# Performance work log

Hardware: AMD Instinct MI355X
Metric: run time of the kernel (lower is better)

The kernel has to match this reference:

```python
import jax, jax.numpy as jnp
import numpy as np

B, DIM, HEADS, H, W = 4, 64, 8, 512, 512


def _conv(x, w, groups=1):
    # NCHW x, OIHW w, stride 1, SAME padding (padding=k//2 in torch)
    return jax.lax.conv_general_dilated(
        x, w, (1, 1), 'SAME', feature_group_count=groups,
        dimension_numbers=('NCHW', 'OIHW', 'NCHW'))


def _dwt_haar(x):
    # single-level orthonormal haar on even-sized NCHW input
    a = x[..., 0::2, 0::2]; b = x[..., 0::2, 1::2]
    c = x[..., 1::2, 0::2]; d = x[..., 1::2, 1::2]
    LL = (a + b + c + d) * 0.5
    LH = (-a - b + c + d) * 0.5
    HL = (-a + b - c + d) * 0.5
    HH = (a - b - c + d) * 0.5
    return LL, LH, HL, HH


def _idwt_haar(LL, LH, HL, HH):
    a = (LL - LH - HL + HH) * 0.5
    b = (LL - LH + HL - HH) * 0.5
    c = (LL + LH - HL - HH) * 0.5
    d = (LL + LH + HL + HH) * 0.5
    Bn, C, h, w = LL.shape
    even = jnp.stack([a, b], -1).reshape(Bn, C, h, 2 * w)  # rows 0::2
    odd = jnp.stack([c, d], -1).reshape(Bn, C, h, 2 * w)   # rows 1::2
    return jnp.stack([even, odd], -2).reshape(Bn, C, 2 * h, 2 * w)


def _l2norm(x, eps=1e-12):
    n = jnp.sqrt(jnp.sum(x * x, axis=-1, keepdims=True))
    return x / jnp.maximum(n, eps)


def setup_inputs() -> dict:
    key = jax.random.key(0)
    ks = jax.random.split(key, 8)
    def w(k, shape):
        fan_in = shape[1] * shape[2] * shape[3]
        return jax.random.normal(k, shape, jnp.float32) * (1.0 / np.sqrt(fan_in))
    return {
        'x': jax.random.normal(ks[0], (B, DIM, H, W), jnp.float32),
        'w_hc1': w(ks[1], (2 * DIM, DIM, 3, 3)),        # groups=2 over 2*dim channels
        'w_hc2': w(ks[2], (DIM, 2 * DIM, 1, 1)),
        'w_ho': w(ks[3], (3 * DIM, DIM, 3, 3)),          # groups=3 over 3*dim channels
        'w_qkv': w(ks[4], (3 * DIM, DIM, 1, 1)),
        'w_dw': w(ks[5], (3 * DIM, 1, 3, 3)),            # depthwise, groups=3*dim
        'w_proj': w(ks[6], (DIM, DIM, 1, 1)),
        'temperature': jnp.ones((HEADS, 1, 1), jnp.float32),
    }


def reference(x, w_hc1, w_hc2, w_ho, w_qkv, w_dw, w_proj, temperature):
    LL, LH, HL, HH = _dwt_haar(x)

    # high-frequency (LH,HL) filter branch
    hv = jnp.concatenate([LH, HL], axis=1)
    filter_hv = jax.nn.relu(_conv(jax.nn.relu(_conv(hv, w_hc1, groups=2)), w_hc2))

    # qkv from LL: 1x1 conv then depthwise 3x3
    qkv = _conv(_conv(LL, w_qkv), w_dw, groups=3 * DIM)
    q, k, v = jnp.split(qkv, 3, axis=1)
    b, c, h, w = q.shape
    v = v * filter_hv + v

    ch = c // HEADS
    q = q.reshape(b, HEADS, ch, h * w)
    k = k.reshape(b, HEADS, ch, h * w)
    v = v.reshape(b, HEADS, ch, h * w)
    q = _l2norm(q)
    k = _l2norm(k)

    attn = jnp.einsum('bhcn,bhdn->bhcd', q, k) * temperature  # [b,heads,ch,ch]
    attn = jax.nn.softmax(attn, axis=-1)
    out = jnp.einsum('bhcd,bhdn->bhcn', attn, v).reshape(b, c, h, w)
    out = _conv(out, w_proj)

    # high-frequency output branch
    yh = jax.nn.relu(_conv(jnp.concatenate([LH, HL, HH], axis=1), w_ho, groups=3))
    LH2, HL2, HH2 = jnp.split(yh, 3, axis=1)

    return _idwt_haar(out, LH2, HL2, HH2)
```

## Files before the change

kernel.cpp:

```cpp
#include <hip/hip_runtime.h>
#include <hip/hip_bf16.h>

#define BN 4
#define DIM 64
#define NHEADS 8
#define HH 256
#define WH 256
#define NP (HH*WH)
#define HF 512
#define WF 512

#define PD 258
#define PROW (PD*64)
#define PPLANE ((size_t)PD*PD*64)

typedef __attribute__((ext_vector_type(8))) short bfx8;
typedef __attribute__((ext_vector_type(8))) unsigned short u16x8;
typedef __attribute__((ext_vector_type(4))) unsigned short u16x4;
typedef __attribute__((ext_vector_type(4))) float f32x4;

static __device__ __forceinline__ short f2bf(float f) {
    unsigned u = __float_as_uint(f);
    unsigned r = (u + 0x7FFFu + ((u >> 16) & 1u)) >> 16;
    return (short)r;
}
static __device__ __forceinline__ float bfu(unsigned short u) {
    return __uint_as_float((unsigned)u << 16);
}

__global__ __launch_bounds__(256) void k_setup(unsigned short* __restrict__ tiled16,
                                               const float* __restrict__ w_ho,
                                               const float* __restrict__ w_hc1,
                                               const float* __restrict__ w_hc2,
                                               const float* __restrict__ w_qkv,
                                               short* __restrict__ wrHO,
                                               short* __restrict__ wrHC1,
                                               short* __restrict__ wrHC2,
                                               short* __restrict__ wrQKV) {
    int bx = blockIdx.x, tid = threadIdx.x;
    if (bx < 16) {
        char* base = (char*)(tiled16 + (size_t)bx * PPLANE);
        const int ROWB = PROW * 2;
        for (int k = tid; k < 8224; k += 256) {
            char* dst;
            if (k < 2064) dst = base + (size_t)k * 16;
            else if (k < 4128) dst = base + (size_t)257 * ROWB + (size_t)(k - 2064) * 16;
            else if (k < 6176) { int r = (k - 4128) >> 3, s = (k - 4128) & 7;
                dst = base + (size_t)(r + 1) * ROWB + (size_t)s * 16; }
            else { int r = (k - 6176) >> 3, s = (k - 6176) & 7;
                dst = base + (size_t)(r + 1) * ROWB + 257 * 128 + (size_t)s * 16; }
            *(uint4*)dst = (uint4){0, 0, 0, 0};
        }
        return;
    }
    if (bx < 16 + 432 + 288) {
        const float* w = (bx < 448) ? w_ho : w_hc1;
        short* wrep = (bx < 448) ? wrHO : wrHC1;
        int t = (bx - ((bx < 448) ? 16 : 448)) * 256 + tid;
        unsigned g   = (unsigned)t / 36864u;
        unsigned r1  = (unsigned)t % 36864u;
        unsigned tap = r1 / 4096u;
        unsigned r2  = r1 % 4096u;
        unsigned icb = r2 / 512u;
        unsigned r3  = r2 % 512u;
        unsigned oc  = r3 >> 3;
        unsigned j   = r3 & 7u;
        wrep[t] = f2bf(w[(((size_t)g * 64 + oc) * 64 + icb * 8u + j) * 9 + tap]);
        return;
    }
    if (bx < 16 + 432 + 288 + 32) {
        int t = (bx - 736) * 256 + tid;
        int j = t & 7, gr = t >> 3, o16 = gr & 15, X = gr >> 4;
        int icb = X % 16, oct = X / 16;
        wrHC2[t] = f2bf(w_hc2[(size_t)(oct * 16 + o16) * 128 + icb * 8 + j]);
        return;
    }
    {
        int t = (bx - 768) * 256 + tid;
        int j = t & 7, gr = t >> 3, o16 = gr & 15, X = gr >> 4;
        int icb = X % 8, oct = X / 8;
        wrQKV[t] = f2bf(w_qkv[(size_t)(oct * 16 + o16) * 64 + icb * 8 + j]);
    }
}

__global__ __launch_bounds__(256) void k_dwt(const float* __restrict__ x,
                                             unsigned short* __restrict__ tiled,
                                             unsigned short* __restrict__ llp) {
    __shared__ unsigned short lds[3 * 128 * 64] __attribute__((aligned(16)));
    const int tid = threadIdx.x;
    const int pid = blockIdx.x;
    const int b = blockIdx.y;
    const int y0 = (pid >> 4) * 8, x0 = (pid & 15) * 16;
    const int quad = tid & 127;
    const int qy = quad >> 4, qx = quad & 15;
    const int gy = y0 + qy, gx = x0 + qx;
    const int ich = tid >> 7;
    unsigned short* llb = llp + (size_t)b * PPLANE + ((size_t)(gy + 1) * PD + (gx + 1)) * 64;

#pragma unroll 4
    for (int it = 0; it < 16; ++it) {
        int ic = it * 4 + ich * 2;
        unsigned g = (((unsigned)(ic >> 3)) + (unsigned)gx + 2u * (unsigned)gy) & 7u;
        unsigned swz = (unsigned)quad * 64 + (g << 3) + (unsigned)(ic & 7);
        unsigned pk[3], pll;
#pragma unroll
        for (int s = 0; s < 2; ++s) {
            const float* px = x + (((size_t)(b * 64 + ic + s) * HF) + 2 * gy) * WF + 2 * gx;
            float2 e0 = *(const float2*)px;
            float2 e1 = *(const float2*)(px + WF);
            float a = e0.x, bb = e0.y, c = e1.x, d = e1.y;
            unsigned ll = (unsigned short)f2bf(( a + bb + c + d) * 0.5f);
            unsigned lh = (unsigned short)f2bf((-a - bb + c + d) * 0.5f);
            unsigned hl = (unsigned short)f2bf((-a + bb - c + d) * 0.5f);
            unsigned hh = (unsigned short)f2bf(( a - bb - c + d) * 0.5f);
            if (s == 0) { pll = ll; pk[0] = lh; pk[1] = hl; pk[2] = hh; }
            else { pll |= ll << 16; pk[0] |= lh << 16; pk[1] |= hl << 16; pk[2] |= hh << 16; }
        }
        *(unsigned*)&lds[swz]          = pk[0];
        *(unsigned*)&lds[8192 + swz]   = pk[1];
        *(unsigned*)&lds[16384 + swz]  = pk[2];
        *(unsigned*)&llb[(g << 3) + (unsigned)(ic & 7)] = pll;
    }
    __syncthreads();
#pragma unroll
    for (int it = 0; it < 12; ++it) {
        int cch = tid + it * 256;
        int p = cch >> 10, rem = cch & 1023;
        int row = rem >> 7, col = rem & 127;
        unsigned short* dst = tiled + ((size_t)(b * 3 + p) * PD + (y0 + row + 1)) * PROW
                                    + (size_t)(x0 + 1) * 64 + (size_t)col * 8;
        *(uint4*)dst = *(const uint4*)((const char*)lds + (size_t)cch * 16);
    }
}

template <int LAYOUT>
__global__ __launch_bounds__(256) void k_gconv3x3_mfma(const unsigned short* __restrict__ tiled,
                                                       const bfx8* __restrict__ wr,
                                                       unsigned short* __restrict__ out, int OC) {
    __shared__ short lds_in[324 * 64] __attribute__((aligned(16)));
    const int tid = threadIdx.x;
    const int l = tid & 63, wv = tid >> 6;
    const int tile = blockIdx.x;
    const int x0 = (tile & 15) * 16, y0 = (tile >> 4) * 16;
    const int g = blockIdx.y, b = blockIdx.z;
    const unsigned short* src = tiled + (size_t)(b * 3 + g) * PPLANE;

#pragma unroll
    for (int it = 0; it < 10; ++it) {
        int cch = it * 256 + tid;
        unsigned row = (unsigned)cch / 144u, col = (unsigned)cch % 144u;
        const unsigned short* ga = src + (size_t)(y0 + row) * PROW + (size_t)x0 * 64 + (size_t)col * 8;
        __builtin_amdgcn_global_load_lds(
            (const __attribute__((address_space(1))) void*)ga,
            (__attribute__((address_space(3))) void*)((char*)lds_in + (size_t)(it * 256 + wv * 64) * 16),
            16, 0, 0);
    }
    if (tid < 32) {
        int cch = 2560 + tid;
        unsigned row = (unsigned)cch / 144u, col = (unsigned)cch % 144u;
        const unsigned short* ga = src + (size_t)(y0 + row) * PROW + (size_t)x0 * 64 + (size_t)col * 8;
        *(uint4*)((char*)lds_in + (size_t)cch * 16) = *(const uint4*)ga;
    }
    __syncthreads();

    f32x4 acc[4][4];
#pragma unroll
    for (int i = 0; i < 4; ++i)
#pragma unroll
        for (int j = 0; j < 4; ++j) acc[i][j] = (f32x4){0.f, 0.f, 0.f, 0.f};

    const int lx = l & 15, lq = l >> 4;
#pragma unroll
    for (int c = 0; c < 2; ++c) {
        const int icb = c * 4 + lq;
#pragma unroll
        for (int tap = 0; tap < 9; ++tap) {
            const int dy = tap / 3, dx = tap % 3;
            const size_t wbase = ((size_t)(g * 9 + tap) * 8 + icb) * 64 + lx;
            bfx8 b0 = wr[wbase];
            bfx8 b1 = wr[wbase + 16];
            bfx8 b2 = wr[wbase + 32];
            bfx8 b3 = wr[wbase + 48];
#pragma unroll
            for (int pg = 0; pg < 4; ++pg) {
                int hy = wv * 4 + pg + dy, hx = lx + dx;
                int hp = hy * 18 + hx;
                const bfx8* ap = (const bfx8*)&lds_in[hp * 64 + (((icb + hx + 2 * hy + 5) & 7) << 3)];
                bfx8 a = *ap;
                acc[pg][0] = __builtin_amdgcn_mfma_f32_16x16x32_bf16(a, b0, acc[pg][0], 0, 0, 0);
                acc[pg][1] = __builtin_amdgcn_mfma_f32_16x16x32_bf16(a, b1, acc[pg][1], 0, 0, 0);
                acc[pg][2] = __builtin_amdgcn_mfma_f32_16x16x32_bf16(a, b2, acc[pg][2], 0, 0, 0);
                acc[pg][3] = __builtin_amdgcn_mfma_f32_16x16x32_bf16(a, b3, acc[pg][3], 0, 0, 0);
            }
        }
    }

#pragma unroll
    for (int pg = 0; pg < 4; ++pg) {
#pragma unroll
        for (int ocg = 0; ocg < 4; ++ocg) {
            f32x4 v = acc[pg][ocg];
            if (LAYOUT == 0) {
                unsigned short* op = out + ((size_t)(b * 256 + tile) * OC + g * 64 + ocg * 16 + lx) * 256
                                         + (wv * 4 + pg) * 16 + lq * 4;
                ushort4 s4;
                s4.x = (unsigned short)f2bf(fmaxf(v.x, 0.f));
                s4.y = (unsigned short)f2bf(fmaxf(v.y, 0.f));
                s4.z = (unsigned short)f2bf(fmaxf(v.z, 0.f));
                s4.w = (unsigned short)f2bf(fmaxf(v.w, 0.f));
                *(ushort4*)op = s4;
            } else {
                int icT = g * 64 + ocg * 16 + lx;
                int g16 = icT >> 3;
                unsigned short* tb = out + ((size_t)(b * 256 + tile) * 256) * 128;
                int innerb = (wv * 4 + pg) * 16 + lq * 4;
                float vr[4] = {v.x, v.y, v.z, v.w};
#pragma unroll
                for (int r = 0; r < 4; ++r) {
                    int inn = innerb + r;
                    tb[(size_t)inn * 128 + (((g16 + inn) & 15) << 3) + (icT & 7)] =
                        (unsigned short)f2bf(fmaxf(vr[r], 0.f));
                }
            }
        }
    }
}

template <int CIN, int OC, bool RELU>
__global__ __launch_bounds__(256) void k_conv1x1_mfma(const unsigned short* __restrict__ inT,
                                                      const bfx8* __restrict__ wr,
                                                      unsigned short* __restrict__ out) {
    constexpr int KB = CIN / 8;
    constexpr int KC = CIN / 32;
    constexpr int NOCT = OC / 16;
    __shared__ short ldsA[256 * CIN] __attribute__((aligned(16)));
    const int tid = threadIdx.x;
    const int l = tid & 63, wv = tid >> 6;
    const int tile = blockIdx.x, b = blockIdx.y;
    const unsigned short* src = inT + ((size_t)(b * 256 + tile) * 256) * CIN;
    constexpr int ITER = (256 * CIN / 8) / 256;
#pragma unroll
    for (int it = 0; it < ITER; ++it) {
        int cc = it * 256 + tid;
        __builtin_amdgcn_global_load_lds(
            (const __attribute__((address_space(1))) void*)(src + (size_t)cc * 8),
            (__attribute__((address_space(3))) void*)((char*)ldsA + (size_t)(it * 256 + wv * 64) * 16),
            16, 0, 0);
    }
    __syncthreads();

    const int lx = l & 15, lq = l >> 4;
    const int x0 = (tile & 15) * 16, y0 = (tile >> 4) * 16;
#pragma unroll
    for (int o4 = 0; o4 < NOCT / 4; ++o4) {
        f32x4 acc[4][4];
#pragma unroll
        for (int i = 0; i < 4; ++i)
#pragma unroll
            for (int j = 0; j < 4; ++j) acc[i][j] = (f32x4){0.f, 0.f, 0.f, 0.f};
#pragma unroll
        for (int c = 0; c < KC; ++c) {
            const int icb = c * 4 + lq;
            bfx8 bf[4];
#pragma unroll
            for (int ot = 0; ot < 4; ++ot)
                bf[ot] = wr[(size_t)(((o4 * 4 + ot) * KB + icb) * 16) + lx];
#pragma unroll
            for (int pg = 0; pg < 4; ++pg) {
                int inner = (wv * 4 + pg) * 16 + lx;
                const bfx8* ap = (const bfx8*)&ldsA[inner * CIN + (((icb + inner) & (KB - 1)) << 3)];
                bfx8 a = *ap;
                acc[pg][0] = __builtin_amdgcn_mfma_f32_16x16x32_bf16(a, bf[0], acc[pg][0], 0, 0, 0);
                acc[pg][1] = __builtin_amdgcn_mfma_f32_16x16x32_bf16(a, bf[1], acc[pg][1], 0, 0, 0);
                acc[pg][2] = __builtin_amdgcn_mfma_f32_16x16x32_bf16(a, bf[2], acc[pg][2], 0, 0, 0);
                acc[pg][3] = __builtin_amdgcn_mfma_f32_16x16x32_bf16(a, bf[3], acc[pg][3], 0, 0, 0);
            }
        }
#pragma unroll
        for (int pg = 0; pg < 4; ++pg)
#pragma unroll
            for (int ot = 0; ot < 4; ++ot) {
                int oc = (o4 * 4 + ot) * 16 + lx;
                unsigned short* op = out + ((size_t)b * OC + oc) * NP
                                         + (size_t)(y0 + wv * 4 + pg) * WH + x0 + lq * 4;
                f32x4 v = acc[pg][ot];
                ushort4 s4;
                s4.x = (unsigned short)f2bf(RELU ? fmaxf(v.x, 0.f) : v.x);
                s4.y = (unsigned short)f2bf(RELU ? fmaxf(v.y, 0.f) : v.y);
                s4.z = (unsigned short)f2bf(RELU ? fmaxf(v.z, 0.f) : v.z);
                s4.w = (unsigned short)f2bf(RELU ? fmaxf(v.w, 0.f) : v.w);
                *(ushort4*)op = s4;
            }
    }
}

__global__ __launch_bounds__(256) void k_qkv_fused(const unsigned short* __restrict__ llp,
                                                   const bfx8* __restrict__ wrq,
                                                   const float* __restrict__ wdw,
                                                   const unsigned short* __restrict__ filt,
                                                   unsigned short* __restrict__ vt,
                                                   float* __restrict__ praw,
                                                   float* __restrict__ praw2) {
    __shared__ short ldsA[336 * 64] __attribute__((aligned(16)));
    __shared__ short qsave[64 * 256] __attribute__((aligned(16)));
    __shared__ float ssq[2][4][64];
    const int tid = threadIdx.x;
    const int l = tid & 63, wv = tid >> 6;
    const int tile = blockIdx.x, b = blockIdx.y;
    const int x0 = (tile & 15) * 16, y0 = (tile >> 4) * 16;
    const unsigned short* src = llp + (size_t)b * PPLANE;

#pragma unroll
    for (int it = 0; it < 10; ++it) {
        int cch = it * 256 + tid;
        unsigned row = (unsigned)cch / 144u, col = (unsigned)cch % 144u;
        const unsigned short* ga = src + (size_t)(y0 + row) * PROW + (size_t)x0 * 64 + (size_t)col * 8;
        __builtin_amdgcn_global_load_lds(
            (const __attribute__((address_space(1))) void*)ga,
            (__attribute__((address_space(3))) void*)((char*)ldsA + (size_t)(it * 256 + wv * 64) * 16),
            16, 0, 0);
    }
    if (tid < 32) {
        int cch = 2560 + tid;
        unsigned row = (unsigned)cch / 144u, col = (unsigned)cch % 144u;
        const unsigned short* ga = src + (size_t)(y0 + row) * PROW + (size_t)x0 * 64 + (size_t)col * 8;
        *(uint4*)((char*)ldsA + (size_t)cch * 16) = *(const uint4*)ga;
    }
    __syncthreads();

    const int lx = l & 15, lq = l >> 4;
    bfx8 af[6][2];
#pragma unroll
    for (int m = 0; m < 6; ++m) {
        int mt = wv + 4 * m;
        if (mt < 21) {
            int hp = mt * 16 + lx;
            int hy = hp / 18, hx = hp - hy * 18;
#pragma unroll
            for (int kc = 0; kc < 2; ++kc) {
                int icb = kc * 4 + lq;
                af[m][kc] = *(const bfx8*)&ldsA[hp * 64 + (((icb + hx + 2 * hy + 5) & 7) << 3)];
            }
        }
    }
    __syncthreads();

    for (int g3 = 0; g3 < 3; ++g3) {
        bfx8 bw[2][4];
#pragma unroll
        for (int kc = 0; kc < 2; ++kc)
#pragma unroll
            for (int nt = 0; nt < 4; ++nt)
                bw[kc][nt] = wrq[(size_t)(((g3 * 4 + nt) * 8) + kc * 4 + lq) * 16 + lx];
#pragma unroll
        for (int m = 0; m < 6; ++m) {
            int mt = wv + 4 * m;
            if (mt < 21) {
                f32x4 acc[4];
#pragma unroll
                for (int nt = 0; nt < 4; ++nt) acc[nt] = (f32x4){0.f, 0.f, 0.f, 0.f};
#pragma unroll
                for (int kc = 0; kc < 2; ++kc) {
                    bfx8 a = af[m][kc];
#pragma unroll
                    for (int nt = 0; nt < 4; ++nt)
                        acc[nt] = __builtin_amdgcn_mfma_f32_16x16x32_bf16(a, bw[kc][nt], acc[nt], 0, 0, 0);
                }
#pragma unroll
                for (int nt = 0; nt < 4; ++nt) {
                    int ocl = nt * 16 + lx;
                    float vr[4] = {acc[nt].x, acc[nt].y, acc[nt].z, acc[nt].w};
#pragma unroll
                    for (int r = 0; r < 4; ++r) {
                        int hp2 = mt * 16 + lq * 4 + r;
                        int hy2 = hp2 / 18, hx2 = hp2 - hy2 * 18;
                        ldsA[hp2 * 64 + ((((ocl >> 3) + hx2 + 2 * hy2) & 7) << 3) + (ocl & 7)] =
                            f2bf(vr[r]);
                    }
                }
            }
        }
        __syncthreads();
        const int ch = l, chg = g3 * 64 + ch;
        float w9[9];
#pragma unroll
        for (int t = 0; t < 9; ++t) w9[t] = wdw[chg * 9 + t];
        float s2 = 0.f;
        u16x8 kpk[4][2];
#pragma unroll
        for (int yy = 0; yy < 4; ++yy) {
            int y = wv * 4 + yy;
            float ln[3][18];
#pragma unroll
            for (int hr = 0; hr < 3; ++hr) {
                int hy = y + hr;
#pragma unroll
                for (int hx = 0; hx < 18; ++hx)
                    ln[hr][hx] = bfu((unsigned short)ldsA[(hy * 18 + hx) * 64 +
                                     ((((ch >> 3) + hx + 2 * hy) & 7) << 3) + (ch & 7)]);
            }
            float ox[16];
#pragma unroll
            for (int xx = 0; xx < 16; ++xx) {
                float s = 0.f;
#pragma unroll
                for (int hr = 0; hr < 3; ++hr)
#pragma unroll
                    for (int dx = 0; dx < 3; ++dx)
                        s = fmaf(ln[hr][xx + dx], w9[hr * 3 + dx], s);
                ox[xx] = s;
            }
            if (g3 == 2) {
                const unsigned short* fp = filt + ((size_t)b * 64 + ch) * NP
                                                + (size_t)(y0 + y) * WH + x0;
                u16x8 f0 = *(const u16x8*)fp;
                u16x8 f1 = *(const u16x8*)(fp + 8);
#pragma unroll
                for (int k = 0; k < 8; ++k) ox[k]     = fmaf(ox[k],     bfu(f0[k]), ox[k]);
#pragma unroll
                for (int k = 0; k < 8; ++k) ox[8 + k] = fmaf(ox[8 + k], bfu(f1[k]), ox[8 + k]);
                unsigned short* vb = vt + ((size_t)(b * 256 + tile) * 256 + (size_t)y * 16) * 64 + ch;
#pragma unroll
                for (int xx = 0; xx < 16; ++xx) vb[xx * 64] = (unsigned short)f2bf(ox[xx]);
            } else {
#pragma unroll
                for (int xx = 0; xx < 16; ++xx) s2 = fmaf(ox[xx], ox[xx], s2);
                if (g3 == 0) {
#pragma unroll
                    for (int xx = 0; xx < 16; ++xx) {
                        int px = y * 16 + xx;
                        qsave[ch * 256 + ((((px >> 3) + ch) & 31) << 3) + (px & 7)] =
                            f2bf(ox[xx]);
                    }
                } else {
#pragma unroll
                    for (int xx = 0; xx < 8; ++xx)  kpk[yy][0][xx] = (unsigned short)f2bf(ox[xx]);
#pragma unroll
                    for (int xx = 0; xx < 8; ++xx)  kpk[yy][1][xx] = (unsigned short)f2bf(ox[8 + xx]);
                }
            }
        }
        if (g3 == 0) ssq[0][wv][ch] = s2;
        if (g3 == 1) {
            ssq[1][wv][ch] = s2;
            __syncthreads();
            short* kbuf = ldsA;
#pragma unroll
            for (int yy = 0; yy < 4; ++yy) {
                int y = wv * 4 + yy;
#pragma unroll
                for (int xx = 0; xx < 16; ++xx) {
                    int px = y * 16 + xx;
                    kbuf[ch * 256 + ((((px >> 3) + ch) & 31) << 3) + (px & 7)] =
                        (short)kpk[yy][xx >> 3][xx & 7];
                }
            }
            __syncthreads();
            f32x4 sacc[4];
#pragma unroll
            for (int t16 = 0; t16 < 4; ++t16) sacc[t16] = (f32x4){0.f, 0.f, 0.f, 0.f};
#pragma unroll
            for (int kc2 = 0; kc2 < 2; ++kc2) {
                int kc = wv * 2 + kc2;
#pragma unroll
                for (int t16 = 0; t16 < 4; ++t16) {
                    int chh = t16 * 16 + lx;
                    int go = chh * 256 + (((kc * 4 + lq + chh) & 31) << 3);
                    bfx8 aq = *(const bfx8*)&qsave[go];
                    bfx8 bk = *(const bfx8*)&kbuf[go];
                    sacc[t16] = __builtin_amdgcn_mfma_f32_16x16x32_bf16(aq, bk, sacc[t16], 0, 0, 0);
                }
            }
            __syncthreads();
            float* sred = (float*)qsave;
#pragma unroll
            for (int t16 = 0; t16 < 4; ++t16)
                *(f32x4*)&sred[((wv * 4 + t16) * 64 + l) * 4] = sacc[t16];
            __syncthreads();
            {
                int t16r = tid >> 6, lr = tid & 63;
                f32x4 s0 = *(const f32x4*)&sred[((0 * 4 + t16r) * 64 + lr) * 4];
                f32x4 s1 = *(const f32x4*)&sred[((1 * 4 + t16r) * 64 + lr) * 4];
                f32x4 s2r = *(const f32x4*)&sred[((2 * 4 + t16r) * 64 + lr) * 4];
                f32x4 s3 = *(const f32x4*)&sred[((3 * 4 + t16r) * 64 + lr) * 4];
                f32x4 sum = s0 + s1 + s2r + s3;
                *(f32x4*)&praw[(((size_t)(b * 256 + tile) * 4 + t16r) * 64 + lr) * 4] = sum;
                if (tid < 128) {
                    int which = tid >> 6, chh = tid & 63;
                    praw2[(size_t)(b * 256 + tile) * 128 + tid] =
                        ssq[which][0][chh] + ssq[which][1][chh] +
                        ssq[which][2][chh] + ssq[which][3][chh];
                }
            }
        }
        __syncthreads();
    }
}

__global__ __launch_bounds__(64) void k_attn_soft(const float* __restrict__ praw,
                                                  const float* __restrict__ praw2,
                                                  const float* __restrict__ temp,
                                                  float* __restrict__ attn) {
    int bhd = blockIdx.x;
    int b = bhd >> 3, hd = bhd & 7;
    int t = threadIdx.x, c = t >> 3, d = t & 7;
    int t16 = hd >> 1, half = hd & 1;
    int cl = half * 8 + c, dl = half * 8 + d;
    const float* pb = praw + ((size_t)(b * 256) * 4 + t16) * 256 + ((cl >> 2) * 16 + dl) * 4 + (cl & 3);
    const float* p2 = praw2 + (size_t)(b * 256) * 128;
    float s = 0.f, sq = 0.f, sk = 0.f;
    for (int tile = 0; tile < 256; ++tile) {
        s  += pb[(size_t)tile * 1024];
        sq += p2[(size_t)tile * 128 + hd * 8 + c];
        sk += p2[(size_t)tile * 128 + 64 + hd * 8 + d];
    }
    float nq = fmaxf(sqrtf(sq), 1e-12f);
    float nk = fmaxf(sqrtf(sk), 1e-12f);
    s = s / (nq * nk) * temp[hd];
    __shared__ float sm[64];
    __shared__ float se[64];
    sm[t] = s;
    __syncthreads();
    float mx = -1e30f;
#pragma unroll
    for (int dd = 0; dd < 8; ++dd) mx = fmaxf(mx, sm[c * 8 + dd]);
    float e = __expf(s - mx);
    se[t] = e;
    __syncthreads();
    float sum = 0.f;
#pragma unroll
    for (int dd = 0; dd < 8; ++dd) sum += se[c * 8 + dd];
    attn[(size_t)bhd * 64 + t] = e / sum;
}

__global__ __launch_bounds__(256) void k_prep_attn(const float* __restrict__ attn,
                                                   const float* __restrict__ wproj,
                                                   short* __restrict__ mrep) {
    int b = blockIdx.x, t = threadIdx.x;
    const float* ab = attn + (size_t)b * 512;
#pragma unroll
    for (int i = 0; i < 16; ++i) {
        int idx = t * 16 + i;
        int j = idx & 7, o16 = (idx >> 3) & 15, icb = (idx >> 7) & 7, oct = idx >> 10;
        int oc = oct * 16 + o16;
        float m = 0.f;
#pragma unroll
        for (int c8 = 0; c8 < 8; ++c8)
            m = fmaf(wproj[(size_t)oc * 64 + icb * 8 + c8], ab[icb * 64 + c8 * 8 + j], m);
        mrep[(size_t)b * 4096 + idx] = f2bf(m);
    }
}

__global__ __launch_bounds__(256) void k_attnout_idwt(const unsigned short* __restrict__ vt,
                                                      const bfx8* __restrict__ mrep,
                                                      const unsigned short* __restrict__ yht,
                                                      float* __restrict__ out) {
    const int tid = threadIdx.x;
    const int l = tid & 63, wv = tid >> 6;
    const int lx = l & 15, lq = l >> 4;
    const int tile = blockIdx.x, b = blockIdx.y;
    const int x0 = (tile & 15) * 16, y0 = (tile >> 4) * 16;
    const bfx8* vtb = (const bfx8*)(vt + (size_t)(b * 256 + tile) * 256 * 64);
    const bfx8* mb = mrep + (size_t)b * 512;

    bfx8 bw[2][4];
#pragma unroll
    for (int kc = 0; kc < 2; ++kc)
#pragma unroll
        for (int nt = 0; nt < 4; ++nt)
            bw[kc][nt] = mb[(nt * 8 + kc * 4 + lq) * 16 + lx];

    const unsigned short* yb = yht + (size_t)(b * 256 + tile) * 192 * 256;

#pragma unroll
    for (int pg = 0; pg < 4; ++pg) {
        const int mt = wv * 4 + pg;
        const int y = y0 + mt;
        bfx8 a0 = vtb[(mt * 16 + lx) * 8 + lq];
        bfx8 a1 = vtb[(mt * 16 + lx) * 8 + 4 + lq];

        f32x4 acc[4];
#pragma unroll
        for (int nt = 0; nt < 4; ++nt) acc[nt] = (f32x4){0.f, 0.f, 0.f, 0.f};
#pragma unroll
        for (int nt = 0; nt < 4; ++nt) {
            acc[nt] = __builtin_amdgcn_mfma_f32_16x16x32_bf16(a0, bw[0][nt], acc[nt], 0, 0, 0);
            acc[nt] = __builtin_amdgcn_mfma_f32_16x16x32_bf16(a1, bw[1][nt], acc[nt], 0, 0, 0);
        }
#pragma unroll
        for (int nt = 0; nt < 4; ++nt) {
            const int oc = nt * 16 + lx;
            const int inner = mt * 16 + lq * 4;
            const unsigned short* yp = yb + (size_t)oc * 256 + inner;
            u16x4 lh4 = *(const u16x4*)yp;
            u16x4 hl4 = *(const u16x4*)(yp + (size_t)64 * 256);
            u16x4 hh4 = *(const u16x4*)(yp + (size_t)128 * 256);
            float e0[8], e1[8];
#pragma unroll
            for (int r = 0; r < 4; ++r) {
                float s  = acc[nt][r];
                float LH = bfu(lh4[r]), HL = bfu(hl4[r]), HHv = bfu(hh4[r]);
                e0[2 * r]     = (s - LH - HL + HHv) * 0.5f;
                e0[2 * r + 1] = (s - LH + HL - HHv) * 0.5f;
                e1[2 * r]     = (s + LH - HL - HHv) * 0.5f;
                e1[2 * r + 1] = (s + LH + HL + HHv) * 0.5f;
            }
            float* o0 = out + ((size_t)(b * 64 + oc) * HF + 2 * y) * WF + 2 * (x0 + lq * 4);
            *(float4*)o0            = *(float4*)&e0[0];
            *(float4*)(o0 + 4)      = *(float4*)&e0[4];
            *(float4*)(o0 + WF)     = *(float4*)&e1[0];
            *(float4*)(o0 + WF + 4) = *(float4*)&e1[4];
        }
    }
}

extern "C" void kernel_launch(void* const* d_in, const int* in_sizes, int n_in,
                              void* d_out, int out_size, void* d_ws, size_t ws_size,
                              hipStream_t stream) {
    const float* x      = (const float*)d_in[0];
    const float* w_hc1  = (const float*)d_in[1];
    const float* w_hc2  = (const float*)d_in[2];
    const float* w_ho   = (const float*)d_in[3];
    const float* w_qkv  = (const float*)d_in[4];
    const float* w_dw   = (const float*)d_in[5];
    const float* w_proj = (const float*)d_in[6];
    const float* temp   = (const float*)d_in[7];
    float* out = (float*)d_out;

    char* base = (char*)d_ws;
    unsigned short* TILED = (unsigned short*)(base + 0);
    unsigned short* LLP   = (unsigned short*)(base + 102242304ULL);
    unsigned short* YH    = (unsigned short*)(base + 136323072ULL);
    unsigned short* T1T   = (unsigned short*)(base + 236986368ULL);
    unsigned short* FILT  = (unsigned short*)(base + 304095232ULL);
    unsigned short* VT    = (unsigned short*)(base + 337649664ULL);
    float*          PRAW  = (float*)(base + 371204096ULL);
    float*          PRAW2 = (float*)(base + 375398400ULL);
    float*          ATTN  = (float*)(base + 375922688ULL);
    short* WREP_HO  = (short*)(base + 375930880ULL);
    short* WREP_HC1 = (short*)(base + 376152064ULL);
    short* WREP_HC2 = (short*)(base + 376299520ULL);
    short* WREP_QKV = (short*)(base + 376315904ULL);
    short* MREP     = (short*)(base + 376340480ULL);

    k_setup<<<816, 256, 0, stream>>>(TILED, w_ho, w_hc1, w_hc2, w_qkv,
                                     WREP_HO, WREP_HC1, WREP_HC2, WREP_QKV);
    k_dwt<<<dim3(512, BN), 256, 0, stream>>>(x, TILED, LLP);
    k_gconv3x3_mfma<0><<<dim3(256, 3, BN), 256, 0, stream>>>(TILED, (const bfx8*)WREP_HO, YH, 192);
    k_gconv3x3_mfma<1><<<dim3(256, 2, BN), 256, 0, stream>>>(TILED, (const bfx8*)WREP_HC1, T1T, 128);
    k_conv1x1_mfma<128, 64, true><<<dim3(256, BN), 256, 0, stream>>>(T1T, (const bfx8*)WREP_HC2, FILT);
    k_qkv_fused<<<dim3(256, BN), 256, 0, stream>>>(LLP, (const bfx8*)WREP_QKV, w_dw, FILT,
                                                   VT, PRAW, PRAW2);
    k_attn_soft<<<32, 64, 0, stream>>>(PRAW, PRAW2, temp, ATTN);
    k_prep_attn<<<BN, 256, 0, stream>>>(ATTN, w_proj, MREP);
    k_attnout_idwt<<<dim3(256, BN), 256, 0, stream>>>(VT, (const bfx8*)MREP, YH, out);
}
```

Measured before the change: 563.7 us.

## Fuse high-frequency 3x3 grouped convs and 1x1 filter conv into one kernel

```diff
diff --git a/kernel.cpp b/kernel.cpp
--- a/kernel.cpp
+++ b/kernel.cpp
@@ -133,162 +133,189 @@
     }
 }
 
-template <int LAYOUT>
-__global__ __launch_bounds__(256) void k_gconv3x3_mfma(const unsigned short* __restrict__ tiled,
-                                                       const bfx8* __restrict__ wr,
-                                                       unsigned short* __restrict__ out, int OC) {
-    __shared__ short lds_in[324 * 64] __attribute__((aligned(16)));
+__global__ __launch_bounds__(256) void k_hi_fused(const unsigned short* __restrict__ tiled,
+                                                  const bfx8* __restrict__ wrHO,
+                                                  const bfx8* __restrict__ wrHC1,
+                                                  const bfx8* __restrict__ wrHC2,
+                                                  unsigned short* __restrict__ yh,
+                                                  unsigned short* __restrict__ filt) {
+    __shared__ short halo[324 * 64] __attribute__((aligned(16)));
+    __shared__ short t1A[256 * 64] __attribute__((aligned(16)));
     const int tid = threadIdx.x;
     const int l = tid & 63, wv = tid >> 6;
-    const int tile = blockIdx.x;
+    const int lx = l & 15, lq = l >> 4;
+    const int tile = blockIdx.x, b = blockIdx.y;
     const int x0 = (tile & 15) * 16, y0 = (tile >> 4) * 16;
-    const int g = blockIdx.y, b = blockIdx.z;
-    const unsigned short* src = tiled + (size_t)(b * 3 + g) * PPLANE;
-
-#pragma unroll
-    for (int it = 0; it < 10; ++it) {
-        int cch = it * 256 + tid;
-        unsigned row = (unsigned)cch / 144u, col = (unsigned)cch % 144u;
-        const unsigned short* ga = src + (size_t)(y0 + row) * PROW + (size_t)x0 * 64 + (size_t)col * 8;
-        __builtin_amdgcn_global_load_lds(
-            (const __attribute__((address_space(1))) void*)ga,
-            (__attribute__((address_space(3))) void*)((char*)lds_in + (size_t)(it * 256 + wv * 64) * 16),
-            16, 0, 0);
-    }
-    if (tid < 32) {
-        int cch = 2560 + tid;
-        unsigned row = (unsigned)cch / 144u, col = (unsigned)cch % 144u;
-        const unsigned short* ga = src + (size_t)(y0 + row) * PROW + (size_t)x0 * 64 + (size_t)col * 8;
-        *(uint4*)((char*)lds_in + (size_t)cch * 16) = *(const uint4*)ga;
-    }
-    __syncthreads();
-
-    f32x4 acc[4][4];
-#pragma unroll
-    for (int i = 0; i < 4; ++i)
-#pragma unroll
-        for (int j = 0; j < 4; ++j) acc[i][j] = (f32x4){0.f, 0.f, 0.f, 0.f};
-
-    const int lx = l & 15, lq = l >> 4;
-#pragma unroll
-    for (int c = 0; c < 2; ++c) {
-        const int icb = c * 4 + lq;
-#pragma unroll
-        for (int tap = 0; tap < 9; ++tap) {
-            const int dy = tap / 3, dx = tap % 3;
-            const size_t wbase = ((size_t)(g * 9 + tap) * 8 + icb) * 64 + lx;
-            bfx8 b0 = wr[wbase];
-            bfx8 b1 = wr[wbase + 16];
-            bfx8 b2 = wr[wbase + 32];
-            bfx8 b3 = wr[wbase + 48];
+    const int order[3] = {0, 2, 1};
+
+#pragma unroll
+    for (int ph = 0; ph < 3; ++ph) {
+        const int g = order[ph];
+        const unsigned short* src = tiled + (size_t)(b * 3 + g) * PPLANE;
+#pragma unroll
+        for (int it = 0; it < 10; ++it) {
+            int cch = it * 256 + tid;
+            unsigned row = (unsigned)cch / 144u, col = (unsigned)cch % 144u;
+            const unsigned short* ga = src + (size_t)(y0 + row) * PROW + (size_t)x0 * 64 + (size_t)col * 8;
+            __builtin_amdgcn_global_load_lds(
+                (const __attribute__((address_space(1))) void*)ga,
+                (__attribute__((address_space(3))) void*)((char*)halo + (size_t)(it * 256 + wv * 64) * 16),
+                16, 0, 0);
+        }
+        if (tid < 32) {
+            int cch = 2560 + tid;
+            unsigned row = (unsigned)cch / 144u, col = (unsigned)cch % 144u;
+            const unsigned short* ga = src + (size_t)(y0 + row) * PROW + (size_t)x0 * 64 + (size_t)col * 8;
+            *(uint4*)((char*)halo + (size_t)cch * 16) = *(const uint4*)ga;
+        }
+        __syncthreads();
+
+        {
+            f32x4 acc[4][4];
+#pragma unroll
+            for (int i = 0; i < 4; ++i)
+#pragma unroll
+                for (int j = 0; j < 4; ++j) acc[i][j] = (f32x4){0.f, 0.f, 0.f, 0.f};
+#pragma unroll
+            for (int c = 0; c < 2; ++c) {
+                const int icb = c * 4 + lq;
+#pragma unroll
+                for (int tap = 0; tap < 9; ++tap) {
+                    const int dy = tap / 3, dx = tap % 3;
+                    const size_t wbase = ((size_t)(g * 9 + tap) * 8 + icb) * 64 + lx;
+                    bfx8 b0 = wrHO[wbase];
+                    bfx8 b1 = wrHO[wbase + 16];
+                    bfx8 b2 = wrHO[wbase + 32];
+                    bfx8 b3 = wrHO[wbase + 48];
+#pragma unroll
+                    for (int pg = 0; pg < 4; ++pg) {
+                        int hy = wv * 4 + pg + dy, hx = lx + dx;
+                        int hp = hy * 18 + hx;
+                        bfx8 a = *(const bfx8*)&halo[hp * 64 + (((icb + hx + 2 * hy + 5) & 7) << 3)];
+                        acc[pg][0] = __builtin_amdgcn_mfma_f32_16x16x32_bf16(a, b0, acc[pg][0], 0, 0, 0);
+                        acc[pg][1] = __builtin_amdgcn_mfma_f32_16x16x32_bf16(a, b1, acc[pg][1], 0, 0, 0);
+                        acc[pg][2] = __builtin_amdgcn_mfma_f32_16x16x32_bf16(a, b2, acc[pg][2], 0, 0, 0);
+                        acc[pg][3] = __builtin_amdgcn_mfma_f32_16x16x32_bf16(a, b3, acc[pg][3], 0, 0, 0);
+                    }
+                }
+            }
+#pragma unroll
+            for (int pg = 0; pg < 4; ++pg)
+#pragma unroll
+                for (int ocg = 0; ocg < 4; ++ocg) {
+                    f32x4 v = acc[pg][ocg];
+                    unsigned short* op = yh + ((size_t)(b * 256 + tile) * 192 + g * 64 + ocg * 16 + lx) * 256
+                                            + (wv * 4 + pg) * 16 + lq * 4;
+                    ushort4 s4;
+                    s4.x = (unsigned short)f2bf(fmaxf(v.x, 0.f));
+                    s4.y = (unsigned short)f2bf(fmaxf(v.y, 0.f));
+                    s4.z = (unsigned short)f2bf(fmaxf(v.z, 0.f));
+                    s4.w = (unsigned short)f2bf(fmaxf(v.w, 0.f));
+                    *(ushort4*)op = s4;
+                }
+        }
+
+        if (ph != 1) {
+            f32x4 tacc[4][4];
+#pragma unroll
+            for (int i = 0; i < 4; ++i)
+#pragma unroll
+                for (int j = 0; j < 4; ++j) tacc[i][j] = (f32x4){0.f, 0.f, 0.f, 0.f};
+#pragma unroll
+            for (int c = 0; c < 2; ++c) {
+                const int icb = c * 4 + lq;
+#pragma unroll
+                for (int tap = 0; tap < 9; ++tap) {
+                    const int dy = tap / 3, dx = tap % 3;
+                    const size_t wbase = ((size_t)(g * 9 + tap) * 8 + icb) * 64 + lx;
+                    bfx8 b0 = wrHC1[wbase];
+                    bfx8 b1 = wrHC1[wbase + 16];
+                    bfx8 b2 = wrHC1[wbase + 32];
+                    bfx8 b3 = wrHC1[wbase + 48];
+#pragma unroll
+                    for (int pg = 0; pg < 4; ++pg) {
+                        int hy = wv * 4 + pg + dy, hx = lx + dx;
+                        int hp = hy * 18 + hx;
+                        bfx8 a = *(const bfx8*)&halo[hp * 64 + (((icb + hx + 2 * hy + 5) & 7) << 3)];
+                        tacc[pg][0] = __builtin_amdgcn_mfma_f32_16x16x32_bf16(a, b0, tacc[pg][0], 0, 0, 0);
+                        tacc[pg][1] = __builtin_amdgcn_mfma_f32_16x16x32_bf16(a, b1, tacc[pg][1], 0, 0, 0);
+                        tacc[pg][2] = __builtin_amdgcn_mfma_f32_16x16x32_bf16(a, b2, tacc[pg][2], 0, 0, 0);
+                        tacc[pg][3] = __builtin_amdgcn_mfma_f32_16x16x32_bf16(a, b3, tacc[pg][3], 0, 0, 0);
+                    }
+                }
+            }
+            if (ph == 0) {
+#pragma unroll
+                for (int pg = 0; pg < 4; ++pg)
+#pragma unroll
+                    for (int ocg = 0; ocg < 4; ++ocg) {
+                        int ch = ocg * 16 + lx;
+                        float vr[4] = {tacc[pg][ocg].x, tacc[pg][ocg].y, tacc[pg][ocg].z, tacc[pg][ocg].w};
+#pragma unroll
+                        for (int r = 0; r < 4; ++r) {
+                            int inn = (wv * 4 + pg) * 16 + lq * 4 + r;
+                            t1A[inn * 64 + ((((ch >> 3) + inn) & 7) << 3) + (ch & 7)] =
+                                f2bf(fmaxf(vr[r], 0.f));
+                        }
+                    }
+            } else {
+                __syncthreads();
+#pragma unroll
+                for (int pg = 0; pg < 4; ++pg)
+#pragma unroll
+                    for (int ocg = 0; ocg < 4; ++ocg) {
+                        int ch = ocg * 16 + lx;
+                        float vr[4] = {tacc[pg][ocg].x, tacc[pg][ocg].y, tacc[pg][ocg].z, tacc[pg][ocg].w};
+#pragma unroll
+                        for (int r = 0; r < 4; ++r) {
+                            int inn = (wv * 4 + pg) * 16 + lq * 4 + r;
+                            halo[inn * 64 + ((((ch >> 3) + inn) & 7) << 3) + (ch & 7)] =
+                                f2bf(fmaxf(vr[r], 0.f));
+                        }
+                    }
+            }
+        }
+        __syncthreads();
+    }
+
+    {
+        f32x4 facc[4][4];
+#pragma unroll
+        for (int i = 0; i < 4; ++i)
+#pragma unroll
+            for (int j = 0; j < 4; ++j) facc[i][j] = (f32x4){0.f, 0.f, 0.f, 0.f};
+#pragma unroll
+        for (int c = 0; c < 4; ++c) {
+            const int icb = c * 4 + lq;
+            const int e = icb & 7;
+            const short* abase = (c < 2) ? t1A : halo;
+            bfx8 bf[4];
+#pragma unroll
+            for (int ot = 0; ot < 4; ++ot)
+                bf[ot] = wrHC2[(size_t)((ot * 16 + icb) * 16) + lx];
 #pragma unroll
             for (int pg = 0; pg < 4; ++pg) {
-                int hy = wv * 4 + pg + dy, hx = lx + dx;
-                int hp = hy * 18 + hx;
-                const bfx8* ap = (const bfx8*)&lds_in[hp * 64 + (((icb + hx + 2 * hy + 5) & 7) << 3)];
-                bfx8 a = *ap;
-                acc[pg][0] = __builtin_amdgcn_mfma_f32_16x16x32_bf16(a, b0, acc[pg][0], 0, 0, 0);
-                acc[pg][1] = __builtin_amdgcn_mfma_f32_16x16x32_bf16(a, b1, acc[pg][1], 0, 0, 0);
-                acc[pg][2] = __builtin_amdgcn_mfma_f32_16x16x32_bf16(a, b2, acc[pg][2], 0, 0, 0);
-                acc[pg][3] = __builtin_amdgcn_mfma_f32_16x16x32_bf16(a, b3, acc[pg][3], 0, 0, 0);
-            }
-        }
-    }
-
-#pragma unroll
-    for (int pg = 0; pg < 4; ++pg) {
-#pragma unroll
-        for (int ocg = 0; ocg < 4; ++ocg) {
-            f32x4 v = acc[pg][ocg];
-            if (LAYOUT == 0) {
-                unsigned short* op = out + ((size_t)(b * 256 + tile) * OC + g * 64 + ocg * 16 + lx) * 256
+                int inner = (wv * 4 + pg) * 16 + lx;
+                bfx8 a = *(const bfx8*)&abase[inner * 64 + (((e + inner) & 7) << 3)];
+                facc[pg][0] = __builtin_amdgcn_mfma_f32_16x16x32_bf16(a, bf[0], facc[pg][0], 0, 0, 0);
+                facc[pg][1] = __builtin_amdgcn_mfma_f32_16x16x32_bf16(a, bf[1], facc[pg][1], 0, 0, 0);
+                facc[pg][2] = __builtin_amdgcn_mfma_f32_16x16x32_bf16(a, bf[2], facc[pg][2], 0, 0, 0);
+                facc[pg][3] = __builtin_amdgcn_mfma_f32_16x16x32_bf16(a, bf[3], facc[pg][3], 0, 0, 0);
+            }
+        }
+#pragma unroll
+        for (int pg = 0; pg < 4; ++pg)
+#pragma unroll
+            for (int ot = 0; ot < 4; ++ot) {
+                int oc = ot * 16 + lx;
+                unsigned short* op = filt + ((size_t)(b * 256 + tile) * 64 + oc) * 256
                                          + (wv * 4 + pg) * 16 + lq * 4;
+                f32x4 v = facc[pg][ot];
                 ushort4 s4;
                 s4.x = (unsigned short)f2bf(fmaxf(v.x, 0.f));
                 s4.y = (unsigned short)f2bf(fmaxf(v.y, 0.f));
                 s4.z = (unsigned short)f2bf(fmaxf(v.z, 0.f));
                 s4.w = (unsigned short)f2bf(fmaxf(v.w, 0.f));
-                *(ushort4*)op = s4;
-            } else {
-                int icT = g * 64 + ocg * 16 + lx;
-                int g16 = icT >> 3;
-                unsigned short* tb = out + ((size_t)(b * 256 + tile) * 256) * 128;
-                int innerb = (wv * 4 + pg) * 16 + lq * 4;
-                float vr[4] = {v.x, v.y, v.z, v.w};
-#pragma unroll
-                for (int r = 0; r < 4; ++r) {
-                    int inn = innerb + r;
-                    tb[(size_t)inn * 128 + (((g16 + inn) & 15) << 3) + (icT & 7)] =
-                        (unsigned short)f2bf(fmaxf(vr[r], 0.f));
-                }
-            }
-        }
-    }
-}
-
-template <int CIN, int OC, bool RELU>
-__global__ __launch_bounds__(256) void k_conv1x1_mfma(const unsigned short* __restrict__ inT,
-                                                      const bfx8* __restrict__ wr,
-                                                      unsigned short* __restrict__ out) {
-    constexpr int KB = CIN / 8;
-    constexpr int KC = CIN / 32;
-    constexpr int NOCT = OC / 16;
-    __shared__ short ldsA[256 * CIN] __attribute__((aligned(16)));
-    const int tid = threadIdx.x;
-    const int l = tid & 63, wv = tid >> 6;
-    const int tile = blockIdx.x, b = blockIdx.y;
-    const unsigned short* src = inT + ((size_t)(b * 256 + tile) * 256) * CIN;
-    constexpr int ITER = (256 * CIN / 8) / 256;
-#pragma unroll
-    for (int it = 0; it < ITER; ++it) {
-        int cc = it * 256 + tid;
-        __builtin_amdgcn_global_load_lds(
-            (const __attribute__((address_space(1))) void*)(src + (size_t)cc * 8),
-            (__attribute__((address_space(3))) void*)((char*)ldsA + (size_t)(it * 256 + wv * 64) * 16),
-            16, 0, 0);
-    }
-    __syncthreads();
-
-    const int lx = l & 15, lq = l >> 4;
-    const int x0 = (tile & 15) * 16, y0 = (tile >> 4) * 16;
-#pragma unroll
-    for (int o4 = 0; o4 < NOCT / 4; ++o4) {
-        f32x4 acc[4][4];
-#pragma unroll
-        for (int i = 0; i < 4; ++i)
-#pragma unroll
-            for (int j = 0; j < 4; ++j) acc[i][j] = (f32x4){0.f, 0.f, 0.f, 0.f};
-#pragma unroll
-        for (int c = 0; c < KC; ++c) {
-            const int icb = c * 4 + lq;
-            bfx8 bf[4];
-#pragma unroll
-            for (int ot = 0; ot < 4; ++ot)
-                bf[ot] = wr[(size_t)(((o4 * 4 + ot) * KB + icb) * 16) + lx];
-#pragma unroll
-            for (int pg = 0; pg < 4; ++pg) {
-                int inner = (wv * 4 + pg) * 16 + lx;
-                const bfx8* ap = (const bfx8*)&ldsA[inner * CIN + (((icb + inner) & (KB - 1)) << 3)];
-                bfx8 a = *ap;
-                acc[pg][0] = __builtin_amdgcn_mfma_f32_16x16x32_bf16(a, bf[0], acc[pg][0], 0, 0, 0);
-                acc[pg][1] = __builtin_amdgcn_mfma_f32_16x16x32_bf16(a, bf[1], acc[pg][1], 0, 0, 0);
-                acc[pg][2] = __builtin_amdgcn_mfma_f32_16x16x32_bf16(a, bf[2], acc[pg][2], 0, 0, 0);
-                acc[pg][3] = __builtin_amdgcn_mfma_f32_16x16x32_bf16(a, bf[3], acc[pg][3], 0, 0, 0);
-            }
-        }
-#pragma unroll
-        for (int pg = 0; pg < 4; ++pg)
-#pragma unroll
-            for (int ot = 0; ot < 4; ++ot) {
-                int oc = (o4 * 4 + ot) * 16 + lx;
-                unsigned short* op = out + ((size_t)b * OC + oc) * NP
-                                         + (size_t)(y0 + wv * 4 + pg) * WH + x0 + lq * 4;
-                f32x4 v = acc[pg][ot];
-                ushort4 s4;
-                s4.x = (unsigned short)f2bf(RELU ? fmaxf(v.x, 0.f) : v.x);
-                s4.y = (unsigned short)f2bf(RELU ? fmaxf(v.y, 0.f) : v.y);
-                s4.z = (unsigned short)f2bf(RELU ? fmaxf(v.z, 0.f) : v.z);
-                s4.w = (unsigned short)f2bf(RELU ? fmaxf(v.w, 0.f) : v.w);
                 *(ushort4*)op = s4;
             }
     }
@@ -411,8 +438,7 @@
                 ox[xx] = s;
             }
             if (g3 == 2) {
-                const unsigned short* fp = filt + ((size_t)b * 64 + ch) * NP
-                                                + (size_t)(y0 + y) * WH + x0;
+                const unsigned short* fp = filt + ((size_t)(b * 256 + tile) * 64 + ch) * 256 + y * 16;
                 u16x8 f0 = *(const u16x8*)fp;
                 u16x8 f1 = *(const u16x8*)(fp + 8);
 #pragma unroll
@@ -631,24 +657,23 @@
     unsigned short* TILED = (unsigned short*)(base + 0);
     unsigned short* LLP   = (unsigned short*)(base + 102242304ULL);
     unsigned short* YH    = (unsigned short*)(base + 136323072ULL);
-    unsigned short* T1T   = (unsigned short*)(base + 236986368ULL);
-    unsigned short* FILT  = (unsigned short*)(base + 304095232ULL);
-    unsigned short* VT    = (unsigned short*)(base + 337649664ULL);
-    float*          PRAW  = (float*)(base + 371204096ULL);
-    float*          PRAW2 = (float*)(base + 375398400ULL);
-    float*          ATTN  = (float*)(base + 375922688ULL);
-    short* WREP_HO  = (short*)(base + 375930880ULL);
-    short* WREP_HC1 = (short*)(base + 376152064ULL);
-    short* WREP_HC2 = (short*)(base + 376299520ULL);
-    short* WREP_QKV = (short*)(base + 376315904ULL);
-    short* MREP     = (short*)(base + 376340480ULL);
+    unsigned short* FILT  = (unsigned short*)(base + 236986368ULL);
+    unsigned short* VT    = (unsigned short*)(base + 270540800ULL);
+    float*          PRAW  = (float*)(base + 304095232ULL);
+    float*          PRAW2 = (float*)(base + 308289536ULL);
+    float*          ATTN  = (float*)(base + 308813824ULL);
+    short* WREP_HO  = (short*)(base + 308822016ULL);
+    short* WREP_HC1 = (short*)(base + 309043200ULL);
+    short* WREP_HC2 = (short*)(base + 309190656ULL);
+    short* WREP_QKV = (short*)(base + 309207040ULL);
+    short* MREP     = (short*)(base + 309231616ULL);
 
     k_setup<<<816, 256, 0, stream>>>(TILED, w_ho, w_hc1, w_hc2, w_qkv,
                                      WREP_HO, WREP_HC1, WREP_HC2, WREP_QKV);
     k_dwt<<<dim3(512, BN), 256, 0, stream>>>(x, TILED, LLP);
-    k_gconv3x3_mfma<0><<<dim3(256, 3, BN), 256, 0, stream>>>(TILED, (const bfx8*)WREP_HO, YH, 192);
-    k_gconv3x3_mfma<1><<<dim3(256, 2, BN), 256, 0, stream>>>(TILED, (const bfx8*)WREP_HC1, T1T, 128);
-    k_conv1x1_mfma<128, 64, true><<<dim3(256, BN), 256, 0, stream>>>(T1T, (const bfx8*)WREP_HC2, FILT);
+    k_hi_fused<<<dim3(256, BN), 256, 0, stream>>>(TILED, (const bfx8*)WREP_HO,
+                                                  (const bfx8*)WREP_HC1, (const bfx8*)WREP_HC2,
+                                                  YH, FILT);
     k_qkv_fused<<<dim3(256, BN), 256, 0, stream>>>(LLP, (const bfx8*)WREP_QKV, w_dw, FILT,
                                                    VT, PRAW, PRAW2);
     k_attn_soft<<<32, 64, 0, stream>>>(PRAW, PRAW2, temp, ATTN);
```

New measurement: 604.5 us. 7.2% more time.

## Fuse softmax with projection prep and store FILT in tile-contiguous layout

Applied to the files above, without the earlier changes.

```diff
diff --git a/kernel.cpp b/kernel.cpp
--- a/kernel.cpp
+++ b/kernel.cpp
@@ -250,7 +250,6 @@
     __syncthreads();
 
     const int lx = l & 15, lq = l >> 4;
-    const int x0 = (tile & 15) * 16, y0 = (tile >> 4) * 16;
 #pragma unroll
     for (int o4 = 0; o4 < NOCT / 4; ++o4) {
         f32x4 acc[4][4];
@@ -281,8 +280,8 @@
 #pragma unroll
             for (int ot = 0; ot < 4; ++ot) {
                 int oc = (o4 * 4 + ot) * 16 + lx;
-                unsigned short* op = out + ((size_t)b * OC + oc) * NP
-                                         + (size_t)(y0 + wv * 4 + pg) * WH + x0 + lq * 4;
+                unsigned short* op = out + ((size_t)(b * 256 + tile) * OC + oc) * 256
+                                         + (wv * 4 + pg) * 16 + lq * 4;
                 f32x4 v = acc[pg][ot];
                 ushort4 s4;
                 s4.x = (unsigned short)f2bf(RELU ? fmaxf(v.x, 0.f) : v.x);
@@ -411,8 +410,7 @@
                 ox[xx] = s;
             }
             if (g3 == 2) {
-                const unsigned short* fp = filt + ((size_t)b * 64 + ch) * NP
-                                                + (size_t)(y0 + y) * WH + x0;
+                const unsigned short* fp = filt + ((size_t)(b * 256 + tile) * 64 + ch) * 256 + y * 16;
                 u16x8 f0 = *(const u16x8*)fp;
                 u16x8 f1 = *(const u16x8*)(fp + 8);
 #pragma unroll
@@ -497,15 +495,18 @@
     }
 }
 
-__global__ __launch_bounds__(64) void k_attn_soft(const float* __restrict__ praw,
-                                                  const float* __restrict__ praw2,
-                                                  const float* __restrict__ temp,
-                                                  float* __restrict__ attn) {
-    int bhd = blockIdx.x;
-    int b = bhd >> 3, hd = bhd & 7;
-    int t = threadIdx.x, c = t >> 3, d = t & 7;
-    int t16 = hd >> 1, half = hd & 1;
-    int cl = half * 8 + c, dl = half * 8 + d;
+__global__ __launch_bounds__(512) void k_soft_prep(const float* __restrict__ praw,
+                                                   const float* __restrict__ praw2,
+                                                   const float* __restrict__ temp,
+                                                   const float* __restrict__ wproj,
+                                                   short* __restrict__ mrep) {
+    __shared__ float sm[512];
+    __shared__ float ash[512];
+    const int b = blockIdx.x, tid = threadIdx.x;
+    const int hd = tid >> 6, t = tid & 63;
+    const int c = t >> 3, d = t & 7;
+    const int t16 = hd >> 1, half = hd & 1;
+    const int cl = half * 8 + c, dl = half * 8 + d;
     const float* pb = praw + ((size_t)(b * 256) * 4 + t16) * 256 + ((cl >> 2) * 16 + dl) * 4 + (cl & 3);
     const float* p2 = praw2 + (size_t)(b * 256) * 128;
     float s = 0.f, sq = 0.f, sk = 0.f;
@@ -517,36 +518,30 @@
     float nq = fmaxf(sqrtf(sq), 1e-12f);
     float nk = fmaxf(sqrtf(sk), 1e-12f);
     s = s / (nq * nk) * temp[hd];
-    __shared__ float sm[64];
-    __shared__ float se[64];
-    sm[t] = s;
+    sm[tid] = s;
     __syncthreads();
     float mx = -1e30f;
 #pragma unroll
-    for (int dd = 0; dd < 8; ++dd) mx = fmaxf(mx, sm[c * 8 + dd]);
+    for (int dd = 0; dd < 8; ++dd) mx = fmaxf(mx, sm[hd * 64 + c * 8 + dd]);
     float e = __expf(s - mx);
-    se[t] = e;
+    ash[tid] = e;
     __syncthreads();
     float sum = 0.f;
 #pragma unroll
-    for (int dd = 0; dd < 8; ++dd) sum += se[c * 8 + dd];
-    attn[(size_t)bhd * 64 + t] = e / sum;
-}
-
-__global__ __launch_bounds__(256) void k_prep_attn(const float* __restrict__ attn,
-                                                   const float* __restrict__ wproj,
-                                                   short* __restrict__ mrep) {
-    int b = blockIdx.x, t = threadIdx.x;
-    const float* ab = attn + (size_t)b * 512;
-#pragma unroll
-    for (int i = 0; i < 16; ++i) {
-        int idx = t * 16 + i;
+    for (int dd = 0; dd < 8; ++dd) sum += ash[hd * 64 + c * 8 + dd];
+    float a = e / sum;
+    __syncthreads();
+    ash[tid] = a;
+    __syncthreads();
+#pragma unroll
+    for (int i = 0; i < 8; ++i) {
+        int idx = tid * 8 + i;
         int j = idx & 7, o16 = (idx >> 3) & 15, icb = (idx >> 7) & 7, oct = idx >> 10;
         int oc = oct * 16 + o16;
         float m = 0.f;
 #pragma unroll
         for (int c8 = 0; c8 < 8; ++c8)
-            m = fmaf(wproj[(size_t)oc * 64 + icb * 8 + c8], ab[icb * 64 + c8 * 8 + j], m);
+            m = fmaf(wproj[(size_t)oc * 64 + icb * 8 + c8], ash[icb * 64 + c8 * 8 + j], m);
         mrep[(size_t)b * 4096 + idx] = f2bf(m);
     }
 }
@@ -636,12 +631,11 @@
     unsigned short* VT    = (unsigned short*)(base + 337649664ULL);
     float*          PRAW  = (float*)(base + 371204096ULL);
     float*          PRAW2 = (float*)(base + 375398400ULL);
-    float*          ATTN  = (float*)(base + 375922688ULL);
-    short* WREP_HO  = (short*)(base + 375930880ULL);
-    short* WREP_HC1 = (short*)(base + 376152064ULL);
-    short* WREP_HC2 = (short*)(base + 376299520ULL);
-    short* WREP_QKV = (short*)(base + 376315904ULL);
-    short* MREP     = (short*)(base + 376340480ULL);
+    short* WREP_HO  = (short*)(base + 375922688ULL);
+    short* WREP_HC1 = (short*)(base + 376143872ULL);
+    short* WREP_HC2 = (short*)(base + 376291328ULL);
+    short* WREP_QKV = (short*)(base + 376307712ULL);
+    short* MREP     = (short*)(base + 376332288ULL);
 
     k_setup<<<816, 256, 0, stream>>>(TILED, w_ho, w_hc1, w_hc2, w_qkv,
                                      WREP_HO, WREP_HC1, WREP_HC2, WREP_QKV);
@@ -651,7 +645,6 @@
     k_conv1x1_mfma<128, 64, true><<<dim3(256, BN), 256, 0, stream>>>(T1T, (const bfx8*)WREP_HC2, FILT);
     k_qkv_fused<<<dim3(256, BN), 256, 0, stream>>>(LLP, (const bfx8*)WREP_QKV, w_dw, FILT,
                                                    VT, PRAW, PRAW2);
-    k_attn_soft<<<32, 64, 0, stream>>>(PRAW, PRAW2, temp, ATTN);
-    k_prep_attn<<<BN, 256, 0, stream>>>(ATTN, w_proj, MREP);
+    k_soft_prep<<<BN, 512, 0, stream>>>(PRAW, PRAW2, temp, w_proj, MREP);
     k_attnout_idwt<<<dim3(256, BN), 256, 0, stream>>>(VT, (const bfx8*)MREP, YH, out);
 }
```

Result: no change. 559.2 us (-0.8%).
